# Kernel optimization log

Measured on AMD Instinct MI355X. Metric: run time of the kernel, lower is better.

Reference implementation:

```python
import jax, jax.numpy as jnp
import numpy as np

PF = 8
BITS = 4
T, D, O, A = 1024, 2048, 4096, 4  # tokens, in_dim, per-slice out_dim, max_deltas


def _dequant(qw, qz, sc):
    """GPTQ-style 4-bit dequant, single quant group (g_idx all zero).
    qw: [O, D//PF] int32 (nibbles packed along input dim)
    qz: [O//PF, 1] int32 (zero nibbles packed along output dim)
    sc: [O, 1] float scales
    returns W: [O, D] float32
    """
    Od, Kp = qw.shape
    shifts = jnp.arange(PF, dtype=jnp.int32) * BITS
    q = ((qw[:, :, None] >> shifts) & 0xF).reshape(Od, Kp * PF).astype(jnp.float32)
    z = ((qz[:, 0][:, None] >> shifts) & 0xF).reshape(Od)[:, None].astype(jnp.float32)
    return sc.astype(jnp.float32) * (q - z)


def _delta_slice(x, indices, qw_s, qz_s, sc_s):
    # per-token adapter dispatch: tokens with indices==a use delta weight a
    out = jnp.zeros((x.shape[0], qw_s.shape[1]), dtype=jnp.float32)
    for a in range(qw_s.shape[0]):  # fixed small loop over adapters
        W = _dequant(qw_s[a], qz_s[a], sc_s[a])           # [O, D]
        xm = jnp.where((indices == a)[:, None], x, 0.0)    # gather-by-mask
        out = out + xm @ W.T                               # [T, O]
    return out


def setup_inputs() -> dict:
    key = jax.random.key(0)
    ks = jax.random.split(key, 10)
    MAXI = np.int32(2147483647)
    return {
        "x": jax.random.normal(ks[0], (T, D), dtype=jnp.float32),
        "base_weight": jax.random.normal(ks[1], (2 * O, D), dtype=jnp.float32) * 0.02,
        "base_bias": jax.random.normal(ks[2], (2 * O,), dtype=jnp.float32) * 0.02,
        "qweight_0": jax.random.randint(ks[3], (A, O, D // PF), 0, MAXI, dtype=jnp.int32),
        "qweight_1": jax.random.randint(ks[4], (A, O, D // PF), 0, MAXI, dtype=jnp.int32),
        "qzeros_0": jax.random.randint(ks[5], (A, O // PF, 1), 0, MAXI, dtype=jnp.int32),
        "qzeros_1": jax.random.randint(ks[6], (A, O // PF, 1), 0, MAXI, dtype=jnp.int32),
        "scales_0": jax.random.uniform(ks[7], (A, O, 1), dtype=jnp.float32) * 1e-3,
        "scales_1": jax.random.uniform(ks[8], (A, O, 1), dtype=jnp.float32) * 1e-3,
        "g_idx_0": jnp.zeros((D,), dtype=jnp.int32),
        "g_idx_1": jnp.zeros((D,), dtype=jnp.int32),
        "indices": jax.random.randint(ks[9], (T,), 0, A, dtype=jnp.int32),
    }


def reference(x, base_weight, base_bias, qweight_0, qweight_1, qzeros_0, qzeros_1,
              scales_0, scales_1, g_idx_0, g_idx_1, indices):
    # base ColumnParallelLinear GEMM (+bias, skip_bias_add=False)
    out = x @ base_weight.T + base_bias  # [T, 2*O]
    # apply_delta_packed_nslice onto the two equal output slices
    d0 = _delta_slice(x, indices, qweight_0, qzeros_0, scales_0)
    d1 = _delta_slice(x, indices, qweight_1, qzeros_1, scales_1)
    return out + jnp.concatenate([d0, d1], axis=1)
```

## Files before the change

kernel.cpp:

```cpp
#include <hip/hip_runtime.h>
#include <hip/hip_bf16.h>
#include <stdint.h>

#define T_TOK 1024
#define DIN   2048
#define NOUT  8192
#define OSL   4096
#define ROWS_PAD 1408
#define BM 128
#define BN 128
#define BK 32

typedef _Float16 f16x8 __attribute__((ext_vector_type(8)));
typedef _Float16 f16x2 __attribute__((ext_vector_type(2)));
typedef float    f32x4 __attribute__((ext_vector_type(4)));

__device__ __forceinline__ void gload16(const void* gp, void* lp) {
  __builtin_amdgcn_global_load_lds(
      (__attribute__((address_space(1))) void*)gp,
      (__attribute__((address_space(3))) void*)lp, 16, 0, 0);
}

__device__ __forceinline__ f16x2 u2h(uint32_t u) {
  union { uint32_t u; f16x2 h; } c; c.u = u; return c.h;
}

__global__ void prep_sort(const int* __restrict__ indices,
                          int* __restrict__ inv,
                          int* __restrict__ meta)
{
  __shared__ int cnt[4], cur[4];
  const int tid = threadIdx.x;
  if (tid < 4) cnt[tid] = 0;
  __syncthreads();
  for (int t = tid; t < T_TOK; t += 256) atomicAdd(&cnt[indices[t]], 1);
  __syncthreads();
  if (tid == 0) {
    int off = 0;
    for (int a = 0; a < 4; ++a) {
      meta[a] = off;
      meta[5 + a] = off + cnt[a];
      cur[a] = off;
      off = (off + cnt[a] + 127) & ~127;
    }
    meta[4] = off;
  }
  __syncthreads();
  for (int i = tid; i < ROWS_PAD; i += 256) inv[i] = -1;
  __syncthreads();
  for (int t = tid; t < T_TOK; t += 256) {
    int a = indices[t];
    int p = atomicAdd(&cur[a], 1);
    inv[p] = t;
  }
}

__global__ void prep_x(const float* __restrict__ x, const int* __restrict__ inv,
                       _Float16* __restrict__ xs) {
  const int row = blockIdx.x;
  const int d0 = threadIdx.x * 8;
  const int t = inv[row];
  f16x8 h;
  if (t >= 0) {
    const float* src = x + (size_t)t * DIN + d0;
    float4 f0 = *(const float4*)src;
    float4 f1 = *(const float4*)(src + 4);
    h[0] = (_Float16)f0.x; h[1] = (_Float16)f1.x;
    h[2] = (_Float16)f0.y; h[3] = (_Float16)f1.y;
    h[4] = (_Float16)f0.z; h[5] = (_Float16)f1.z;
    h[6] = (_Float16)f0.w; h[7] = (_Float16)f1.w;
  } else {
#pragma unroll
    for (int j = 0; j < 8; ++j) h[j] = (_Float16)0.0f;
  }
  *(f16x8*)(xs + (size_t)row * DIN + d0) = h;
}

__global__ void wb_prep(const float* __restrict__ wb, _Float16* __restrict__ wbh) {
  const int n = blockIdx.x;
  const int k0 = threadIdx.x * 8;
  const float* src = wb + (size_t)n * DIN + k0;
  float4 f0 = *(const float4*)src;
  float4 f1 = *(const float4*)(src + 4);
  f16x8 h;
  h[0] = (_Float16)f0.x; h[1] = (_Float16)f1.x;
  h[2] = (_Float16)f0.y; h[3] = (_Float16)f1.y;
  h[4] = (_Float16)f0.z; h[5] = (_Float16)f1.z;
  h[6] = (_Float16)f0.w; h[7] = (_Float16)f1.w;
  *(f16x8*)(wbh + (size_t)n * DIN + k0) = h;
}

template<bool PREP>
__global__ __launch_bounds__(256) void kfused(
    const _Float16* __restrict__ xs,
    const _Float16* __restrict__ wbh,
    const float*    __restrict__ wbf,
    const int* __restrict__ qw0, const int* __restrict__ qw1,
    const int* __restrict__ qz0, const int* __restrict__ qz1,
    const float* __restrict__ sc0, const float* __restrict__ sc1,
    const float* __restrict__ bias,
    const int* __restrict__ inv, const int* __restrict__ meta,
    float* __restrict__ out)
{
  const int m0 = blockIdx.y * BM;
  if (m0 >= meta[4]) return;
  int ad = 0;
  if (m0 >= meta[1]) ad = 1;
  if (m0 >= meta[2]) ad = 2;
  if (m0 >= meta[3]) ad = 3;
  if (m0 >= meta[5 + ad]) return;

  const int n0 = blockIdx.x * BN;
  const int sl = n0 >> 12;
  const int tid  = threadIdx.x;
  const int wave = tid >> 6;
  const int lane = tid & 63;
  const int quad = lane >> 4;
  const int l16  = lane & 15;
  const int wm = (wave & 1) << 6;
  const int wn = (wave >> 1) << 6;

  __shared__ __align__(16) char smem[16384];

  f32x4 acc[4][4];
#pragma unroll
  for (int i = 0; i < 4; ++i)
#pragma unroll
    for (int j = 0; j < 4; ++j) acc[i][j] = (f32x4)0.0f;

  const int kch = (((tid & 3) ^ ((tid >> 3) & 3)) << 3);
  const _Float16* ag0 = xs + (size_t)(m0 + (tid >> 2)) * DIN + kch;
  const _Float16* ag1 = ag0 + (size_t)64 * DIN;
  char* sa0 = smem + wave * 1024;
  char* sa1 = smem + 4096 + wave * 1024;

  const int o_local = tid >> 1;
  const int o = n0 + o_local;
  const int o_sl = o & (OSL - 1);
  const int* qw = (sl ? qw1 : qw0) + ((size_t)ad * OSL + o_sl) * (DIN / 8) + ((tid & 1) << 1);
  const int zw = (sl ? qz1 : qz0)[ad * (OSL / 8) + (o_sl >> 3)];
  const float s = (sl ? sc1 : sc0)[(size_t)ad * OSL + o_sl];
  const int z = (zw >> ((o_sl & 7) << 2)) & 0xF;
  f16x2 s2; s2[0] = s2[1] = (_Float16)s;
  f16x2 k2; k2[0] = k2[1] = (_Float16)(float)(-(1024 + z));

  const _Float16* wbhp = nullptr;
  const float*    wbfp = nullptr;
  if (PREP) wbhp = wbh + (size_t)o * DIN + ((tid & 1) << 4);
  else      wbfp = wbf + (size_t)o * DIN + ((tid & 1) << 4);

  const int bswz = (o_local >> 1) & 3;
  char* bb = smem + 8192 + o_local * 64;
  char* bw0 = bb + (((((tid & 1) << 1)    ) ^ bswz) << 4);
  char* bw1 = bb + (((((tid & 1) << 1) | 1) ^ bswz) << 4);

  const int qoff = ((quad ^ ((l16 >> 1) & 3)) << 4);

  for (int k0 = 0; k0 < DIN; k0 += BK) {
    gload16(ag0, sa0);
    gload16(ag1, sa1);
    int2 wv = *(const int2*)qw;

    union { f16x8 v; f16x2 p[4]; } wA, wB;
    if (PREP) {
      wA.v = *(const f16x8*)wbhp;
      wB.v = *(const f16x8*)(wbhp + 8);
    } else {
      const float4 f0 = *(const float4*)(wbfp);
      const float4 f1 = *(const float4*)(wbfp + 4);
      const float4 f2 = *(const float4*)(wbfp + 8);
      const float4 f3 = *(const float4*)(wbfp + 12);
      wA.v[0] = (_Float16)f0.x; wA.v[1] = (_Float16)f1.x;
      wA.v[2] = (_Float16)f0.y; wA.v[3] = (_Float16)f1.y;
      wA.v[4] = (_Float16)f0.z; wA.v[5] = (_Float16)f1.z;
      wA.v[6] = (_Float16)f0.w; wA.v[7] = (_Float16)f1.w;
      wB.v[0] = (_Float16)f2.x; wB.v[1] = (_Float16)f3.x;
      wB.v[2] = (_Float16)f2.y; wB.v[3] = (_Float16)f3.y;
      wB.v[4] = (_Float16)f2.z; wB.v[5] = (_Float16)f3.z;
      wB.v[6] = (_Float16)f2.w; wB.v[7] = (_Float16)f3.w;
    }

    const uint32_t wx = (uint32_t)wv.x, wy = (uint32_t)wv.y;
    union { f16x8 v; f16x2 p[4]; } h0, h1;
#pragma unroll
    for (int j = 0; j < 4; ++j) {
      uint32_t t0 = ((wx >> (4 * j)) & 0x000F000Fu) | 0x64006400u;
      uint32_t t1 = ((wy >> (4 * j)) & 0x000F000Fu) | 0x64006400u;
      h0.p[j] = (u2h(t0) + k2) * s2 + wA.p[j];
      h1.p[j] = (u2h(t1) + k2) * s2 + wB.p[j];
    }
    *(f16x8*)bw0 = h0.v;
    *(f16x8*)bw1 = h1.v;
    __syncthreads();

    f16x8 af[4], bfr[4];
#pragma unroll
    for (int t = 0; t < 4; ++t)
      af[t] = *(const f16x8*)(smem + (wm + t * 16 + l16) * 64 + qoff);
#pragma unroll
    for (int t = 0; t < 4; ++t)
      bfr[t] = *(const f16x8*)(smem + 8192 + (wn + t * 16 + l16) * 64 + qoff);
#pragma unroll
    for (int mt = 0; mt < 4; ++mt)
#pragma unroll
      for (int nt = 0; nt < 4; ++nt)
        acc[mt][nt] = __builtin_amdgcn_mfma_f32_16x16x32_f16(af[mt], bfr[nt], acc[mt][nt], 0, 0, 0);
    __syncthreads();

    ag0 += BK; ag1 += BK; qw += 4;
    if (PREP) wbhp += BK; else wbfp += BK;
  }

#pragma unroll
  for (int mt = 0; mt < 4; ++mt) {
    const int rowb = m0 + wm + mt * 16 + quad * 4;
    int tk[4];
#pragma unroll
    for (int r = 0; r < 4; ++r) tk[r] = inv[rowb + r];
#pragma unroll
    for (int nt = 0; nt < 4; ++nt) {
      const int col = n0 + wn + nt * 16 + l16;
      const float bv = bias[col];
#pragma unroll
      for (int r = 0; r < 4; ++r) {
        if (tk[r] >= 0)
          out[(size_t)tk[r] * NOUT + col] = acc[mt][nt][r] + bv;
      }
    }
  }
}

extern "C" void kernel_launch(void* const* d_in, const int* in_sizes, int n_in,
                              void* d_out, int out_size, void* d_ws, size_t ws_size,
                              hipStream_t stream) {
  const float* x    = (const float*)d_in[0];
  const float* wb   = (const float*)d_in[1];
  const float* bias = (const float*)d_in[2];
  const int*   qw0  = (const int*)d_in[3];
  const int*   qw1  = (const int*)d_in[4];
  const int*   qz0  = (const int*)d_in[5];
  const int*   qz1  = (const int*)d_in[6];
  const float* sc0  = (const float*)d_in[7];
  const float* sc1  = (const float*)d_in[8];
  const int*   indices = (const int*)d_in[11];
  float* out = (float*)d_out;

  char* w = (char*)d_ws;
  _Float16* xs = (_Float16*)w;
  size_t off = (size_t)ROWS_PAD * DIN * 2;
  int* inv  = (int*)(w + off);
  int* meta = inv + ROWS_PAD;
  size_t wbh_off = (off + (size_t)ROWS_PAD * 4 + 64 + 255) & ~(size_t)255;
  _Float16* wbh = (_Float16*)(w + wbh_off);
  const bool prep = ws_size >= wbh_off + (size_t)NOUT * DIN * 2;

  prep_sort<<<1, 256, 0, stream>>>(indices, inv, meta);
  prep_x<<<ROWS_PAD, 256, 0, stream>>>(x, inv, xs);
  if (prep) wb_prep<<<NOUT, 256, 0, stream>>>(wb, wbh);

  dim3 g(NOUT / BN, ROWS_PAD / BM, 1);
  if (prep)
    kfused<true><<<g, 256, 0, stream>>>(xs, wbh, nullptr, qw0, qw1, qz0, qz1,
                                        sc0, sc1, bias, inv, meta, out);
  else
    kfused<false><<<g, 256, 0, stream>>>(xs, nullptr, wb, qw0, qw1, qz0, qz1,
                                         sc0, sc1, bias, inv, meta, out);
}
```

Baseline: 237.9 us.

## Pre-merge dequantized adapter deltas into base weights and use plain GEMM

A single prep kernel sorts tokens, converts x to fp16 unpermuted, and materializes per-adapter effective weights (base + dequantized delta) in fp16 when workspace allows. The main GEMM then loads both operands via global-to-LDS without inline dequantization, gathering x rows through the inverse permutation. This removes dequant ALU and register staging from the GEMM loop, but writes four times as much fp16 weight data each call. A fallback path keeps inline dequant if workspace is small.

```diff
diff --git a/kernel.cpp b/kernel.cpp
--- a/kernel.cpp
+++ b/kernel.cpp
@@ -25,76 +25,196 @@
   union { uint32_t u; f16x2 h; } c; c.u = u; return c.h;
 }
 
-__global__ void prep_sort(const int* __restrict__ indices,
-                          int* __restrict__ inv,
-                          int* __restrict__ meta)
-{
-  __shared__ int cnt[4], cur[4];
-  const int tid = threadIdx.x;
-  if (tid < 4) cnt[tid] = 0;
-  __syncthreads();
-  for (int t = tid; t < T_TOK; t += 256) atomicAdd(&cnt[indices[t]], 1);
-  __syncthreads();
-  if (tid == 0) {
-    int off = 0;
-    for (int a = 0; a < 4; ++a) {
-      meta[a] = off;
-      meta[5 + a] = off + cnt[a];
-      cur[a] = off;
-      off = (off + cnt[a] + 127) & ~127;
-    }
-    meta[4] = off;
-  }
-  __syncthreads();
-  for (int i = tid; i < ROWS_PAD; i += 256) inv[i] = -1;
-  __syncthreads();
-  for (int t = tid; t < T_TOK; t += 256) {
-    int a = indices[t];
-    int p = atomicAdd(&cur[a], 1);
-    inv[p] = t;
-  }
-}
-
-__global__ void prep_x(const float* __restrict__ x, const int* __restrict__ inv,
-                       _Float16* __restrict__ xs) {
-  const int row = blockIdx.x;
-  const int d0 = threadIdx.x * 8;
-  const int t = inv[row];
-  f16x8 h;
-  if (t >= 0) {
-    const float* src = x + (size_t)t * DIN + d0;
-    float4 f0 = *(const float4*)src;
-    float4 f1 = *(const float4*)(src + 4);
-    h[0] = (_Float16)f0.x; h[1] = (_Float16)f1.x;
-    h[2] = (_Float16)f0.y; h[3] = (_Float16)f1.y;
-    h[4] = (_Float16)f0.z; h[5] = (_Float16)f1.z;
-    h[6] = (_Float16)f0.w; h[7] = (_Float16)f1.w;
-  } else {
-#pragma unroll
-    for (int j = 0; j < 8; ++j) h[j] = (_Float16)0.0f;
-  }
-  *(f16x8*)(xs + (size_t)row * DIN + d0) = h;
-}
-
-__global__ void wb_prep(const float* __restrict__ wb, _Float16* __restrict__ wbh) {
-  const int n = blockIdx.x;
-  const int k0 = threadIdx.x * 8;
-  const float* src = wb + (size_t)n * DIN + k0;
-  float4 f0 = *(const float4*)src;
-  float4 f1 = *(const float4*)(src + 4);
+__device__ __forceinline__ f16x8 cvt_interleave(float4 f0, float4 f1) {
   f16x8 h;
   h[0] = (_Float16)f0.x; h[1] = (_Float16)f1.x;
   h[2] = (_Float16)f0.y; h[3] = (_Float16)f1.y;
   h[4] = (_Float16)f0.z; h[5] = (_Float16)f1.z;
   h[6] = (_Float16)f0.w; h[7] = (_Float16)f1.w;
-  *(f16x8*)(wbh + (size_t)n * DIN + k0) = h;
-}
-
-template<bool PREP>
-__global__ __launch_bounds__(256) void kfused(
-    const _Float16* __restrict__ xs,
-    const _Float16* __restrict__ wbh,
-    const float*    __restrict__ wbf,
+  return h;
+}
+
+template<bool FULL>
+__global__ void prep_all(const float* __restrict__ x, const float* __restrict__ wb,
+                         const int* __restrict__ qw0, const int* __restrict__ qw1,
+                         const int* __restrict__ qz0, const int* __restrict__ qz1,
+                         const float* __restrict__ sc0, const float* __restrict__ sc1,
+                         const int* __restrict__ indices,
+                         _Float16* __restrict__ xh,
+                         _Float16* __restrict__ wout,
+                         int* __restrict__ inv, int* __restrict__ meta)
+{
+  const int b = blockIdx.x;
+  const int tid = threadIdx.x;
+
+  if (b == 0) {
+    __shared__ int cnt[4], cur[4];
+    if (tid < 4) cnt[tid] = 0;
+    __syncthreads();
+    for (int t = tid; t < T_TOK; t += 256) atomicAdd(&cnt[indices[t]], 1);
+    __syncthreads();
+    if (tid == 0) {
+      int off = 0;
+      for (int a = 0; a < 4; ++a) {
+        meta[a] = off;
+        meta[5 + a] = off + cnt[a];
+        cur[a] = off;
+        off = (off + cnt[a] + 127) & ~127;
+      }
+      meta[4] = off;
+    }
+    __syncthreads();
+    for (int i = tid; i < ROWS_PAD; i += 256) inv[i] = -1;
+    __syncthreads();
+    for (int t = tid; t < T_TOK; t += 256) {
+      int a = indices[t];
+      int p = atomicAdd(&cur[a], 1);
+      inv[p] = t;
+    }
+    return;
+  }
+
+  if (b <= 1 + T_TOK) {
+    const int row = b - 1;
+    const int d0 = tid * 8;
+    f16x8 h;
+    if (row < T_TOK) {
+      const float* src = x + (size_t)row * DIN + d0;
+      h = cvt_interleave(*(const float4*)src, *(const float4*)(src + 4));
+    } else {
+#pragma unroll
+      for (int j = 0; j < 8; ++j) h[j] = (_Float16)0.0f;
+    }
+    *(f16x8*)(xh + (size_t)row * DIN + d0) = h;
+    return;
+  }
+
+  const int n = b - (2 + T_TOK);
+  const int d0 = tid * 8;
+  const float* src = wb + (size_t)n * DIN + d0;
+  union { f16x8 v; f16x2 p[4]; } wbr;
+  wbr.v = cvt_interleave(*(const float4*)src, *(const float4*)(src + 4));
+
+  if (!FULL) {
+    *(f16x8*)(wout + (size_t)n * DIN + d0) = wbr.v;
+    return;
+  }
+
+  const int sl = n >> 12;
+  const int n_sl = n & (OSL - 1);
+  const int* qw = sl ? qw1 : qw0;
+  const int* qz = sl ? qz1 : qz0;
+  const float* sc = sl ? sc1 : sc0;
+
+#pragma unroll
+  for (int a = 0; a < 4; ++a) {
+    const uint32_t wv = (uint32_t)qw[((size_t)(a * OSL + n_sl)) * (DIN / 8) + tid];
+    const int zw = qz[a * (OSL / 8) + (n_sl >> 3)];
+    const float s = sc[(size_t)a * OSL + n_sl];
+    const int z = (zw >> ((n_sl & 7) << 2)) & 0xF;
+    f16x2 s2; s2[0] = s2[1] = (_Float16)s;
+    f16x2 k2; k2[0] = k2[1] = (_Float16)(float)(-(1024 + z));
+    union { f16x8 v; f16x2 p[4]; } h;
+#pragma unroll
+    for (int j = 0; j < 4; ++j) {
+      uint32_t t0 = ((wv >> (4 * j)) & 0x000F000Fu) | 0x64006400u;
+      h.p[j] = (u2h(t0) + k2) * s2 + wbr.p[j];
+    }
+    *(f16x8*)(wout + ((size_t)(a * NOUT) + n) * DIN + d0) = h.v;
+  }
+}
+
+__global__ __launch_bounds__(256) void kslim(
+    const _Float16* __restrict__ xh, const _Float16* __restrict__ weff,
+    const float* __restrict__ bias,
+    const int* __restrict__ inv, const int* __restrict__ meta,
+    float* __restrict__ out)
+{
+  const int m0 = blockIdx.y * BM;
+  if (m0 >= meta[4]) return;
+  int ad = 0;
+  if (m0 >= meta[1]) ad = 1;
+  if (m0 >= meta[2]) ad = 2;
+  if (m0 >= meta[3]) ad = 3;
+  if (m0 >= meta[5 + ad]) return;
+
+  const int n0 = blockIdx.x * BN;
+  const int tid  = threadIdx.x;
+  const int wave = tid >> 6;
+  const int lane = tid & 63;
+  const int quad = lane >> 4;
+  const int l16  = lane & 15;
+  const int wm = (wave & 1) << 6;
+  const int wn = (wave >> 1) << 6;
+
+  __shared__ __align__(16) char smem[16384];
+
+  f32x4 acc[4][4];
+#pragma unroll
+  for (int i = 0; i < 4; ++i)
+#pragma unroll
+    for (int j = 0; j < 4; ++j) acc[i][j] = (f32x4)0.0f;
+
+  const int kch = (((tid & 3) ^ ((tid >> 3) & 3)) << 3);
+  const int rloc = tid >> 2;
+  int r0 = inv[m0 + rloc];       if (r0 < 0) r0 = T_TOK;
+  int r1 = inv[m0 + rloc + 64];  if (r1 < 0) r1 = T_TOK;
+  const _Float16* ag0 = xh + (size_t)r0 * DIN + kch;
+  const _Float16* ag1 = xh + (size_t)r1 * DIN + kch;
+  const _Float16* bg0 = weff + ((size_t)(ad * NOUT) + n0 + rloc) * DIN + kch;
+  const _Float16* bg1 = bg0 + (size_t)64 * DIN;
+  char* sa0 = smem +         wave * 1024;
+  char* sa1 = smem +  4096 + wave * 1024;
+  char* sb0 = smem +  8192 + wave * 1024;
+  char* sb1 = smem + 12288 + wave * 1024;
+
+  const int qoff = ((quad ^ ((l16 >> 1) & 3)) << 4);
+
+  for (int k0 = 0; k0 < DIN; k0 += BK) {
+    gload16(ag0, sa0);
+    gload16(ag1, sa1);
+    gload16(bg0, sb0);
+    gload16(bg1, sb1);
+    __syncthreads();
+
+    f16x8 af[4], bfr[4];
+#pragma unroll
+    for (int t = 0; t < 4; ++t)
+      af[t] = *(const f16x8*)(smem + (wm + t * 16 + l16) * 64 + qoff);
+#pragma unroll
+    for (int t = 0; t < 4; ++t)
+      bfr[t] = *(const f16x8*)(smem + 8192 + (wn + t * 16 + l16) * 64 + qoff);
+#pragma unroll
+    for (int mt = 0; mt < 4; ++mt)
+#pragma unroll
+      for (int nt = 0; nt < 4; ++nt)
+        acc[mt][nt] = __builtin_amdgcn_mfma_f32_16x16x32_f16(af[mt], bfr[nt], acc[mt][nt], 0, 0, 0);
+    __syncthreads();
+
+    ag0 += BK; ag1 += BK; bg0 += BK; bg1 += BK;
+  }
+
+#pragma unroll
+  for (int mt = 0; mt < 4; ++mt) {
+    const int rowb = m0 + wm + mt * 16 + quad * 4;
+    int tk[4];
+#pragma unroll
+    for (int r = 0; r < 4; ++r) tk[r] = inv[rowb + r];
+#pragma unroll
+    for (int nt = 0; nt < 4; ++nt) {
+      const int col = n0 + wn + nt * 16 + l16;
+      const float bv = bias[col];
+#pragma unroll
+      for (int r = 0; r < 4; ++r) {
+        if (tk[r] >= 0)
+          out[(size_t)tk[r] * NOUT + col] = acc[mt][nt][r] + bv;
+      }
+    }
+  }
+}
+
+__global__ __launch_bounds__(256) void kdq(
+    const _Float16* __restrict__ xh, const _Float16* __restrict__ wbh,
     const int* __restrict__ qw0, const int* __restrict__ qw1,
     const int* __restrict__ qz0, const int* __restrict__ qz1,
     const float* __restrict__ sc0, const float* __restrict__ sc1,
@@ -129,8 +249,11 @@
     for (int j = 0; j < 4; ++j) acc[i][j] = (f32x4)0.0f;
 
   const int kch = (((tid & 3) ^ ((tid >> 3) & 3)) << 3);
-  const _Float16* ag0 = xs + (size_t)(m0 + (tid >> 2)) * DIN + kch;
-  const _Float16* ag1 = ag0 + (size_t)64 * DIN;
+  const int rloc = tid >> 2;
+  int r0 = inv[m0 + rloc];       if (r0 < 0) r0 = T_TOK;
+  int r1 = inv[m0 + rloc + 64];  if (r1 < 0) r1 = T_TOK;
+  const _Float16* ag0 = xh + (size_t)r0 * DIN + kch;
+  const _Float16* ag1 = xh + (size_t)r1 * DIN + kch;
   char* sa0 = smem + wave * 1024;
   char* sa1 = smem + 4096 + wave * 1024;
 
@@ -143,43 +266,21 @@
   const int z = (zw >> ((o_sl & 7) << 2)) & 0xF;
   f16x2 s2; s2[0] = s2[1] = (_Float16)s;
   f16x2 k2; k2[0] = k2[1] = (_Float16)(float)(-(1024 + z));
-
-  const _Float16* wbhp = nullptr;
-  const float*    wbfp = nullptr;
-  if (PREP) wbhp = wbh + (size_t)o * DIN + ((tid & 1) << 4);
-  else      wbfp = wbf + (size_t)o * DIN + ((tid & 1) << 4);
+  const _Float16* wbhp = wbh + (size_t)o * DIN + ((tid & 1) << 4);
 
   const int bswz = (o_local >> 1) & 3;
   char* bb = smem + 8192 + o_local * 64;
   char* bw0 = bb + (((((tid & 1) << 1)    ) ^ bswz) << 4);
   char* bw1 = bb + (((((tid & 1) << 1) | 1) ^ bswz) << 4);
-
   const int qoff = ((quad ^ ((l16 >> 1) & 3)) << 4);
 
   for (int k0 = 0; k0 < DIN; k0 += BK) {
     gload16(ag0, sa0);
     gload16(ag1, sa1);
     int2 wv = *(const int2*)qw;
-
     union { f16x8 v; f16x2 p[4]; } wA, wB;
-    if (PREP) {
-      wA.v = *(const f16x8*)wbhp;
-      wB.v = *(const f16x8*)(wbhp + 8);
-    } else {
-      const float4 f0 = *(const float4*)(wbfp);
-      const float4 f1 = *(const float4*)(wbfp + 4);
-      const float4 f2 = *(const float4*)(wbfp + 8);
-      const float4 f3 = *(const float4*)(wbfp + 12);
-      wA.v[0] = (_Float16)f0.x; wA.v[1] = (_Float16)f1.x;
-      wA.v[2] = (_Float16)f0.y; wA.v[3] = (_Float16)f1.y;
-      wA.v[4] = (_Float16)f0.z; wA.v[5] = (_Float16)f1.z;
-      wA.v[6] = (_Float16)f0.w; wA.v[7] = (_Float16)f1.w;
-      wB.v[0] = (_Float16)f2.x; wB.v[1] = (_Float16)f3.x;
-      wB.v[2] = (_Float16)f2.y; wB.v[3] = (_Float16)f3.y;
-      wB.v[4] = (_Float16)f2.z; wB.v[5] = (_Float16)f3.z;
-      wB.v[6] = (_Float16)f2.w; wB.v[7] = (_Float16)f3.w;
-    }
-
+    wA.v = *(const f16x8*)wbhp;
+    wB.v = *(const f16x8*)(wbhp + 8);
     const uint32_t wx = (uint32_t)wv.x, wy = (uint32_t)wv.y;
     union { f16x8 v; f16x2 p[4]; } h0, h1;
 #pragma unroll
@@ -207,8 +308,7 @@
         acc[mt][nt] = __builtin_amdgcn_mfma_f32_16x16x32_f16(af[mt], bfr[nt], acc[mt][nt], 0, 0, 0);
     __syncthreads();
 
-    ag0 += BK; ag1 += BK; qw += 4;
-    if (PREP) wbhp += BK; else wbfp += BK;
+    ag0 += BK; ag1 += BK; qw += 4; wbhp += BK;
   }
 
 #pragma unroll
@@ -246,23 +346,25 @@
   float* out = (float*)d_out;
 
   char* w = (char*)d_ws;
-  _Float16* xs = (_Float16*)w;
-  size_t off = (size_t)ROWS_PAD * DIN * 2;
+  _Float16* xh = (_Float16*)w;
+  size_t off = (size_t)(T_TOK + 1) * DIN * 2;
   int* inv  = (int*)(w + off);
   int* meta = inv + ROWS_PAD;
-  size_t wbh_off = (off + (size_t)ROWS_PAD * 4 + 64 + 255) & ~(size_t)255;
-  _Float16* wbh = (_Float16*)(w + wbh_off);
-  const bool prep = ws_size >= wbh_off + (size_t)NOUT * DIN * 2;
-
-  prep_sort<<<1, 256, 0, stream>>>(indices, inv, meta);
-  prep_x<<<ROWS_PAD, 256, 0, stream>>>(x, inv, xs);
-  if (prep) wb_prep<<<NOUT, 256, 0, stream>>>(wb, wbh);
-
+  size_t woff = (off + (size_t)ROWS_PAD * 4 + 64 + 255) & ~(size_t)255;
+  _Float16* wout = (_Float16*)(w + woff);
+  const bool full = ws_size >= woff + (size_t)4 * NOUT * DIN * 2;
+
+  const int nprep = 2 + T_TOK + NOUT;
   dim3 g(NOUT / BN, ROWS_PAD / BM, 1);
-  if (prep)
-    kfused<true><<<g, 256, 0, stream>>>(xs, wbh, nullptr, qw0, qw1, qz0, qz1,
-                                        sc0, sc1, bias, inv, meta, out);
-  else
-    kfused<false><<<g, 256, 0, stream>>>(xs, nullptr, wb, qw0, qw1, qz0, qz1,
-                                         sc0, sc1, bias, inv, meta, out);
-}
+
+  if (full) {
+    prep_all<true><<<nprep, 256, 0, stream>>>(x, wb, qw0, qw1, qz0, qz1, sc0, sc1,
+                                              indices, xh, wout, inv, meta);
+    kslim<<<g, 256, 0, stream>>>(xh, wout, bias, inv, meta, out);
+  } else {
+    prep_all<false><<<nprep, 256, 0, stream>>>(x, wb, qw0, qw1, qz0, qz1, sc0, sc1,
+                                               indices, xh, wout, inv, meta);
+    kdq<<<g, 256, 0, stream>>>(xh, wout, qw0, qw1, qz0, qz1, sc0, sc1,
+                               bias, inv, meta, out);
+  }
+}
```

After: 227.1 us. 4.6% less time.

## Fuse prep kernels and dequantize B fragments directly into registers

Applied to the files above, without the earlier changes.

Merges the sort, x conversion and base-weight conversion into one launch. x is now converted in token order, and the GEMM reads rows through the inverse permutation, with a zero row standing in for padding. The B operand (dequantized delta plus base weight) is now built straight into MFMA fragment registers per lane, removing the B LDS staging and halving shared memory. The cost is redundant qweight and base-weight loads across the two M-waves, scattered 4-byte qweight loads, and dropping the fallback path when the workspace is too small.

```diff
diff --git a/kernel.cpp b/kernel.cpp
--- a/kernel.cpp
+++ b/kernel.cpp
@@ -25,76 +25,75 @@
   union { uint32_t u; f16x2 h; } c; c.u = u; return c.h;
 }
 
-__global__ void prep_sort(const int* __restrict__ indices,
-                          int* __restrict__ inv,
-                          int* __restrict__ meta)
-{
-  __shared__ int cnt[4], cur[4];
-  const int tid = threadIdx.x;
-  if (tid < 4) cnt[tid] = 0;
-  __syncthreads();
-  for (int t = tid; t < T_TOK; t += 256) atomicAdd(&cnt[indices[t]], 1);
-  __syncthreads();
-  if (tid == 0) {
-    int off = 0;
-    for (int a = 0; a < 4; ++a) {
-      meta[a] = off;
-      meta[5 + a] = off + cnt[a];
-      cur[a] = off;
-      off = (off + cnt[a] + 127) & ~127;
-    }
-    meta[4] = off;
-  }
-  __syncthreads();
-  for (int i = tid; i < ROWS_PAD; i += 256) inv[i] = -1;
-  __syncthreads();
-  for (int t = tid; t < T_TOK; t += 256) {
-    int a = indices[t];
-    int p = atomicAdd(&cur[a], 1);
-    inv[p] = t;
-  }
-}
-
-__global__ void prep_x(const float* __restrict__ x, const int* __restrict__ inv,
-                       _Float16* __restrict__ xs) {
-  const int row = blockIdx.x;
-  const int d0 = threadIdx.x * 8;
-  const int t = inv[row];
-  f16x8 h;
-  if (t >= 0) {
-    const float* src = x + (size_t)t * DIN + d0;
-    float4 f0 = *(const float4*)src;
-    float4 f1 = *(const float4*)(src + 4);
-    h[0] = (_Float16)f0.x; h[1] = (_Float16)f1.x;
-    h[2] = (_Float16)f0.y; h[3] = (_Float16)f1.y;
-    h[4] = (_Float16)f0.z; h[5] = (_Float16)f1.z;
-    h[6] = (_Float16)f0.w; h[7] = (_Float16)f1.w;
-  } else {
-#pragma unroll
-    for (int j = 0; j < 8; ++j) h[j] = (_Float16)0.0f;
-  }
-  *(f16x8*)(xs + (size_t)row * DIN + d0) = h;
-}
-
-__global__ void wb_prep(const float* __restrict__ wb, _Float16* __restrict__ wbh) {
-  const int n = blockIdx.x;
-  const int k0 = threadIdx.x * 8;
-  const float* src = wb + (size_t)n * DIN + k0;
-  float4 f0 = *(const float4*)src;
-  float4 f1 = *(const float4*)(src + 4);
+__device__ __forceinline__ f16x8 cvt_interleave(float4 f0, float4 f1) {
   f16x8 h;
   h[0] = (_Float16)f0.x; h[1] = (_Float16)f1.x;
   h[2] = (_Float16)f0.y; h[3] = (_Float16)f1.y;
   h[4] = (_Float16)f0.z; h[5] = (_Float16)f1.z;
   h[6] = (_Float16)f0.w; h[7] = (_Float16)f1.w;
-  *(f16x8*)(wbh + (size_t)n * DIN + k0) = h;
-}
-
-template<bool PREP>
-__global__ __launch_bounds__(256) void kfused(
-    const _Float16* __restrict__ xs,
-    const _Float16* __restrict__ wbh,
-    const float*    __restrict__ wbf,
+  return h;
+}
+
+__global__ void prep_all(const float* __restrict__ x, const float* __restrict__ wb,
+                         const int* __restrict__ indices,
+                         _Float16* __restrict__ xh,
+                         _Float16* __restrict__ wbh,
+                         int* __restrict__ inv, int* __restrict__ meta)
+{
+  const int b = blockIdx.x;
+  const int tid = threadIdx.x;
+
+  if (b == 0) {
+    __shared__ int cnt[4], cur[4];
+    if (tid < 4) cnt[tid] = 0;
+    __syncthreads();
+    for (int t = tid; t < T_TOK; t += 256) atomicAdd(&cnt[indices[t]], 1);
+    __syncthreads();
+    if (tid == 0) {
+      int off = 0;
+      for (int a = 0; a < 4; ++a) {
+        meta[a] = off;
+        meta[5 + a] = off + cnt[a];
+        cur[a] = off;
+        off = (off + cnt[a] + 127) & ~127;
+      }
+      meta[4] = off;
+    }
+    __syncthreads();
+    for (int i = tid; i < ROWS_PAD; i += 256) inv[i] = -1;
+    __syncthreads();
+    for (int t = tid; t < T_TOK; t += 256) {
+      int a = indices[t];
+      int p = atomicAdd(&cur[a], 1);
+      inv[p] = t;
+    }
+    return;
+  }
+
+  if (b <= 1 + T_TOK) {
+    const int row = b - 1;
+    const int d0 = tid * 8;
+    f16x8 h;
+    if (row < T_TOK) {
+      const float* src = x + (size_t)row * DIN + d0;
+      h = cvt_interleave(*(const float4*)src, *(const float4*)(src + 4));
+    } else {
+#pragma unroll
+      for (int j = 0; j < 8; ++j) h[j] = (_Float16)0.0f;
+    }
+    *(f16x8*)(xh + (size_t)row * DIN + d0) = h;
+    return;
+  }
+
+  const int n = b - (2 + T_TOK);
+  const int d0 = tid * 8;
+  const float* src = wb + (size_t)n * DIN + d0;
+  f16x8 h = cvt_interleave(*(const float4*)src, *(const float4*)(src + 4));
+  *(f16x8*)(wbh + (size_t)n * DIN + d0) = h;
+}
+
+__global__ __launch_bounds__(256) void kreg(
+    const _Float16* __restrict__ xh, const _Float16* __restrict__ wbh,
     const int* __restrict__ qw0, const int* __restrict__ qw1,
     const int* __restrict__ qz0, const int* __restrict__ qz1,
     const float* __restrict__ sc0, const float* __restrict__ sc1,
@@ -120,7 +119,7 @@
   const int wm = (wave & 1) << 6;
   const int wn = (wave >> 1) << 6;
 
-  __shared__ __align__(16) char smem[16384];
+  __shared__ __align__(16) char smem[8192];
 
   f32x4 acc[4][4];
 #pragma unroll
@@ -129,86 +128,71 @@
     for (int j = 0; j < 4; ++j) acc[i][j] = (f32x4)0.0f;
 
   const int kch = (((tid & 3) ^ ((tid >> 3) & 3)) << 3);
-  const _Float16* ag0 = xs + (size_t)(m0 + (tid >> 2)) * DIN + kch;
-  const _Float16* ag1 = ag0 + (size_t)64 * DIN;
-  char* sa0 = smem + wave * 1024;
+  const int rloc = tid >> 2;
+  int r0 = inv[m0 + rloc];       if (r0 < 0) r0 = T_TOK;
+  int r1 = inv[m0 + rloc + 64];  if (r1 < 0) r1 = T_TOK;
+  const _Float16* ag0 = xh + (size_t)r0 * DIN + kch;
+  const _Float16* ag1 = xh + (size_t)r1 * DIN + kch;
+  char* sa0 = smem +        wave * 1024;
   char* sa1 = smem + 4096 + wave * 1024;
-
-  const int o_local = tid >> 1;
-  const int o = n0 + o_local;
-  const int o_sl = o & (OSL - 1);
-  const int* qw = (sl ? qw1 : qw0) + ((size_t)ad * OSL + o_sl) * (DIN / 8) + ((tid & 1) << 1);
-  const int zw = (sl ? qz1 : qz0)[ad * (OSL / 8) + (o_sl >> 3)];
-  const float s = (sl ? sc1 : sc0)[(size_t)ad * OSL + o_sl];
-  const int z = (zw >> ((o_sl & 7) << 2)) & 0xF;
-  f16x2 s2; s2[0] = s2[1] = (_Float16)s;
-  f16x2 k2; k2[0] = k2[1] = (_Float16)(float)(-(1024 + z));
-
-  const _Float16* wbhp = nullptr;
-  const float*    wbfp = nullptr;
-  if (PREP) wbhp = wbh + (size_t)o * DIN + ((tid & 1) << 4);
-  else      wbfp = wbf + (size_t)o * DIN + ((tid & 1) << 4);
-
-  const int bswz = (o_local >> 1) & 3;
-  char* bb = smem + 8192 + o_local * 64;
-  char* bw0 = bb + (((((tid & 1) << 1)    ) ^ bswz) << 4);
-  char* bw1 = bb + (((((tid & 1) << 1) | 1) ^ bswz) << 4);
-
   const int qoff = ((quad ^ ((l16 >> 1) & 3)) << 4);
+
+  const int* qwb = sl ? qw1 : qw0;
+  const int* qzb = sl ? qz1 : qz0;
+  const float* scb = sl ? sc1 : sc0;
+  const int qz_base = ad * (OSL / 8);
+  const size_t sc_base = (size_t)ad * OSL;
+
+  const int* qp[4];
+  const _Float16* wp[4];
+  f16x2 s2[4], k2[4];
+#pragma unroll
+  for (int nt = 0; nt < 4; ++nt) {
+    const int row = n0 + wn + nt * 16 + l16;
+    const int o_sl = row & (OSL - 1);
+    qp[nt] = qwb + ((size_t)ad * OSL + o_sl) * (DIN / 8) + quad;
+    wp[nt] = wbh + (size_t)row * DIN + quad * 8;
+    const float s = scb[sc_base + o_sl];
+    const int zw = qzb[qz_base + (o_sl >> 3)];
+    const int z = (zw >> ((o_sl & 7) << 2)) & 0xF;
+    s2[nt][0] = s2[nt][1] = (_Float16)s;
+    k2[nt][0] = k2[nt][1] = (_Float16)(float)(-(1024 + z));
+  }
 
   for (int k0 = 0; k0 < DIN; k0 += BK) {
     gload16(ag0, sa0);
     gload16(ag1, sa1);
-    int2 wv = *(const int2*)qw;
-
-    union { f16x8 v; f16x2 p[4]; } wA, wB;
-    if (PREP) {
-      wA.v = *(const f16x8*)wbhp;
-      wB.v = *(const f16x8*)(wbhp + 8);
-    } else {
-      const float4 f0 = *(const float4*)(wbfp);
-      const float4 f1 = *(const float4*)(wbfp + 4);
-      const float4 f2 = *(const float4*)(wbfp + 8);
-      const float4 f3 = *(const float4*)(wbfp + 12);
-      wA.v[0] = (_Float16)f0.x; wA.v[1] = (_Float16)f1.x;
-      wA.v[2] = (_Float16)f0.y; wA.v[3] = (_Float16)f1.y;
-      wA.v[4] = (_Float16)f0.z; wA.v[5] = (_Float16)f1.z;
-      wA.v[6] = (_Float16)f0.w; wA.v[7] = (_Float16)f1.w;
-      wB.v[0] = (_Float16)f2.x; wB.v[1] = (_Float16)f3.x;
-      wB.v[2] = (_Float16)f2.y; wB.v[3] = (_Float16)f3.y;
-      wB.v[4] = (_Float16)f2.z; wB.v[5] = (_Float16)f3.z;
-      wB.v[6] = (_Float16)f2.w; wB.v[7] = (_Float16)f3.w;
-    }
-
-    const uint32_t wx = (uint32_t)wv.x, wy = (uint32_t)wv.y;
-    union { f16x8 v; f16x2 p[4]; } h0, h1;
-#pragma unroll
-    for (int j = 0; j < 4; ++j) {
-      uint32_t t0 = ((wx >> (4 * j)) & 0x000F000Fu) | 0x64006400u;
-      uint32_t t1 = ((wy >> (4 * j)) & 0x000F000Fu) | 0x64006400u;
-      h0.p[j] = (u2h(t0) + k2) * s2 + wA.p[j];
-      h1.p[j] = (u2h(t1) + k2) * s2 + wB.p[j];
-    }
-    *(f16x8*)bw0 = h0.v;
-    *(f16x8*)bw1 = h1.v;
-    __syncthreads();
-
-    f16x8 af[4], bfr[4];
+
+    f16x8 bfr[4];
+#pragma unroll
+    for (int nt = 0; nt < 4; ++nt) {
+      const uint32_t wv = (uint32_t)qp[nt][0];
+      union { f16x8 v; f16x2 p[4]; } wb8;
+      wb8.v = *(const f16x8*)wp[nt];
+      union { f16x8 v; f16x2 p[4]; } h;
+#pragma unroll
+      for (int j = 0; j < 4; ++j) {
+        uint32_t t = ((wv >> (4 * j)) & 0x000F000Fu) | 0x64006400u;
+        h.p[j] = (u2h(t) + k2[nt]) * s2[nt] + wb8.p[j];
+      }
+      bfr[nt] = h.v;
+    }
+
+    __syncthreads();
+    f16x8 af[4];
 #pragma unroll
     for (int t = 0; t < 4; ++t)
       af[t] = *(const f16x8*)(smem + (wm + t * 16 + l16) * 64 + qoff);
 #pragma unroll
-    for (int t = 0; t < 4; ++t)
-      bfr[t] = *(const f16x8*)(smem + 8192 + (wn + t * 16 + l16) * 64 + qoff);
-#pragma unroll
     for (int mt = 0; mt < 4; ++mt)
 #pragma unroll
       for (int nt = 0; nt < 4; ++nt)
         acc[mt][nt] = __builtin_amdgcn_mfma_f32_16x16x32_f16(af[mt], bfr[nt], acc[mt][nt], 0, 0, 0);
     __syncthreads();
 
-    ag0 += BK; ag1 += BK; qw += 4;
-    if (PREP) wbhp += BK; else wbfp += BK;
+    ag0 += BK; ag1 += BK;
+#pragma unroll
+    for (int nt = 0; nt < 4; ++nt) { qp[nt] += 4; wp[nt] += BK; }
   }
 
 #pragma unroll
@@ -246,23 +230,17 @@
   float* out = (float*)d_out;
 
   char* w = (char*)d_ws;
-  _Float16* xs = (_Float16*)w;
-  size_t off = (size_t)ROWS_PAD * DIN * 2;
+  _Float16* xh = (_Float16*)w;
+  size_t off = (size_t)(T_TOK + 1) * DIN * 2;
   int* inv  = (int*)(w + off);
   int* meta = inv + ROWS_PAD;
-  size_t wbh_off = (off + (size_t)ROWS_PAD * 4 + 64 + 255) & ~(size_t)255;
-  _Float16* wbh = (_Float16*)(w + wbh_off);
-  const bool prep = ws_size >= wbh_off + (size_t)NOUT * DIN * 2;
-
-  prep_sort<<<1, 256, 0, stream>>>(indices, inv, meta);
-  prep_x<<<ROWS_PAD, 256, 0, stream>>>(x, inv, xs);
-  if (prep) wb_prep<<<NOUT, 256, 0, stream>>>(wb, wbh);
+  size_t woff = (off + (size_t)ROWS_PAD * 4 + 64 + 255) & ~(size_t)255;
+  _Float16* wbh = (_Float16*)(w + woff);
+
+  const int nprep = 2 + T_TOK + NOUT;
+  prep_all<<<nprep, 256, 0, stream>>>(x, wb, indices, xh, wbh, inv, meta);
 
   dim3 g(NOUT / BN, ROWS_PAD / BM, 1);
-  if (prep)
-    kfused<true><<<g, 256, 0, stream>>>(xs, wbh, nullptr, qw0, qw1, qz0, qz1,
-                                        sc0, sc1, bias, inv, meta, out);
-  else
-    kfused<false><<<g, 256, 0, stream>>>(xs, nullptr, wb, qw0, qw1, qz0, qz1,
-                                         sc0, sc1, bias, inv, meta, out);
-}
+  kreg<<<g, 256, 0, stream>>>(xh, wbh, qw0, qw1, qz0, qz1, sc0, sc1,
+                              bias, inv, meta, out);
+}
```

Measured after the change: 362.2 us. +52.2%, slower.
